# Kernel tuning notes

Measured on AMD Instinct MI355X. Metric: run time of the kernel, lower is better.

The kernel has to match this reference:

```python
import jax, jax.numpy as jnp
import numpy as np

T, H = 4096, 2048


def setup_inputs() -> dict:
    key = jax.random.key(0)
    k_a, k_b, k_x = jax.random.split(key, 3)
    # glorot-style init matching the module: uniform(-1,1) * sqrt(2/sum(shape))
    a = jax.random.uniform(k_a, (H,), minval=-1.0, maxval=1.0) * jnp.sqrt(2.0 / H)
    B = jax.random.uniform(k_b, (H, H), minval=-1.0, maxval=1.0) * jnp.sqrt(2.0 / (2 * H))
    x = jax.random.normal(k_x, (T, H), dtype=jnp.float32)
    return {"x": x, "a": a, "B": B}


def reference(x, a, B):
    # x: (T, H); per-timestep s_t = B.T @ x_t  ->  s = x @ B, laid out NCH = (1, H, T)
    Tl, Hl = x.shape
    s = jnp.einsum("th,hk->kt", x, B)[None]  # (1, H, T)
    # depthwise causal kernel: k[h, t] = a[h]**t, time as final dim, flipped for conv
    exponents = jnp.arange(Tl)
    kernel = jnp.power(a[:, None], exponents)          # (H, T)
    kernel_flipped = jnp.flip(kernel, axis=-1)[:, None, :]  # (H, 1, T) OIH
    s_padded = jnp.pad(s, ((0, 0), (0, 0), (Tl - 1, 0)))    # causal left-pad
    conv_out = jax.lax.conv_general_dilated(
        s_padded, kernel_flipped,
        window_strides=(1,), padding="VALID",
        dimension_numbers=("NCH", "OIH", "NCH"),
        feature_group_count=Hl,
    )  # (1, H, T): h_t[h] = sum_{k<=t} a[h]**(t-k) * s_k[h]
    return jnp.transpose(conv_out, (0, 2, 1))  # (1, T, H)
```

## Files before the change

kernel.cpp:

```cpp
#include <hip/hip_runtime.h>
#include <stdint.h>

#define TDIM 4096
#define HDIM 2048

#define BM 256
#define BN 128
#define BK 64
#define NKT (HDIM / BK)
#define AREG  34816
#define PERBUF 51200
#define SSTR   132

typedef short short8 __attribute__((ext_vector_type(8)));
typedef float f32x4 __attribute__((ext_vector_type(4)));

__device__ __forceinline__ uint16_t f2bf(float f) {
  uint32_t u = __builtin_bit_cast(uint32_t, f);
  u += 0x7fffu + ((u >> 16) & 1u);
  return (uint16_t)(u >> 16);
}
__device__ __forceinline__ float bf2f(uint32_t h) {
  uint32_t u = h << 16;
  return __builtin_bit_cast(float, u);
}

__device__ __forceinline__ void async_copy16(const void* gsrc, void* ldst) {
  __builtin_amdgcn_global_load_lds(
      (const __attribute__((address_space(1))) uint32_t*)gsrc,
      (__attribute__((address_space(3))) uint32_t*)ldst,
      16, 0, 0);
}

__global__ void prep(const float* __restrict__ x, const float* __restrict__ B,
                     uint16_t* __restrict__ xb, uint16_t* __restrict__ Bt) {
  __shared__ uint16_t tile[64][68];
  const int t = threadIdx.x;
  if (blockIdx.x < 4096) {
    size_t i = ((size_t)blockIdx.x * 256 + t) * 8;
    float4 v0 = *(const float4*)(x + i);
    float4 v1 = *(const float4*)(x + i + 4);
    union { uint16_t h[8]; uint4 v; } o;
    o.h[0] = f2bf(v0.x); o.h[1] = f2bf(v0.y); o.h[2] = f2bf(v0.z); o.h[3] = f2bf(v0.w);
    o.h[4] = f2bf(v1.x); o.h[5] = f2bf(v1.y); o.h[6] = f2bf(v1.z); o.h[7] = f2bf(v1.w);
    *(uint4*)(xb + i) = o.v;
  } else {
    const int bid = blockIdx.x - 4096;
    const int n0 = (bid & 31) * 64;
    const int k0 = (bid >> 5) * 64;
    {
      const int r  = t >> 4;
      const int c4 = (t & 15) * 4;
#pragma unroll
      for (int i = 0; i < 4; ++i) {
        int rr = r + i * 16;
        float4 v = *(const float4*)&B[(size_t)(k0 + rr) * HDIM + n0 + c4];
        union { uint16_t h[4]; uint2 u; } o;
        o.h[0] = f2bf(v.x); o.h[1] = f2bf(v.y); o.h[2] = f2bf(v.z); o.h[3] = f2bf(v.w);
        *(uint2*)&tile[rr][c4] = o.u;
      }
    }
    __syncthreads();
    {
      const int nr = t >> 2;
      const int kc = (t & 3) * 4;
#pragma unroll
      for (int i = 0; i < 4; ++i) {
        int kk = kc + i * 16;
        union { uint16_t h[4]; uint2 u; } o;
        o.h[0] = tile[kk][nr];     o.h[1] = tile[kk + 1][nr];
        o.h[2] = tile[kk + 2][nr]; o.h[3] = tile[kk + 3][nr];
        *(uint2*)&Bt[(size_t)(n0 + nr) * HDIM + k0 + kk] = o.u;
      }
    }
  }
}

__global__ __launch_bounds__(512, 2) void gemm_scan(
    const uint16_t* __restrict__ A, const uint16_t* __restrict__ Bt,
    const float* __restrict__ a, float* __restrict__ out) {
  __shared__ __align__(16) char lds[2 * PERBUF];

  const int tid  = threadIdx.x;
  const int lane = tid & 63;
  const int wave = tid >> 6;
  const int wm = (wave >> 1) * 64;
  const int wn = (wave & 1) * 64;

  const int flat = blockIdx.y * gridDim.x + blockIdx.x;
  const int logi = (flat & 7) * 32 + (flat >> 3);
  const int m0 = (logi >> 4) * BM;
  const int n0 = (logi & 15) * BN;

  f32x4 acc[4][4] = {};
  f32x4 accw[4] = {};

  const int lr = lane >> 3;
  const int gc = (lane & 7) ^ lr;

  const int fr = lane & 15;
  const int fq = lane >> 4;

  auto issue_tile = [&](int kt2) {
    size_t koff = (size_t)kt2 * (BK * 2);
    char* dst = lds + (kt2 & 1) * PERBUF;
#pragma unroll
    for (int i = 0; i < 4; ++i) {
      int g = wave * 4 + i;
      int row = m0 - 16 + g * 8 + lr;
      if (row < 0) row = 0;
      async_copy16((const char*)A + ((size_t)row * HDIM + gc * 8) * 2 + koff,
                   dst + g * 1024);
    }
    if (wave < 2) {
      int g = 32 + wave;
      int row = m0 - 16 + g * 8 + lr;
      async_copy16((const char*)A + ((size_t)row * HDIM + gc * 8) * 2 + koff,
                   dst + g * 1024);
    }
#pragma unroll
    for (int i = 0; i < 2; ++i) {
      int g = wave * 2 + i;
      int row = n0 + g * 8 + lr;
      async_copy16((const char*)Bt + ((size_t)row * HDIM + gc * 8) * 2 + koff,
                   dst + AREG + g * 1024);
    }
  };

  issue_tile(0);
  for (int kt = 0; kt < NKT; ++kt) {
    if (kt + 1 < NKT) {
      issue_tile(kt + 1);
      if (wave < 2) asm volatile("s_waitcnt vmcnt(7)" ::: "memory");
      else          asm volatile("s_waitcnt vmcnt(6)" ::: "memory");
    } else {
      asm volatile("s_waitcnt vmcnt(0)" ::: "memory");
    }
    asm volatile("s_barrier" ::: "memory");

    const char* base = lds + (kt & 1) * PERBUF;
#pragma unroll
    for (int s = 0; s < 2; ++s) {
      short8 af[4], bfr[4], aw;
#pragma unroll
      for (int im = 0; im < 4; ++im) {
        int row = 16 + wm + im * 16 + fr;
        af[im] = *(const short8*)(base + row * 128 + (((s * 4 + fq) ^ (fr & 7)) * 16));
      }
#pragma unroll
      for (int in = 0; in < 4; ++in) {
        int row = wn + in * 16 + fr;
        bfr[in] = *(const short8*)(base + AREG + row * 128 + (((s * 4 + fq) ^ (fr & 7)) * 16));
      }
#pragma unroll
      for (int im = 0; im < 4; ++im)
#pragma unroll
        for (int in = 0; in < 4; ++in)
          acc[im][in] = __builtin_amdgcn_mfma_f32_16x16x32_bf16(
              af[im], bfr[in], acc[im][in], 0, 0, 0);
      if (wave < 2) {
        aw = *(const short8*)(base + fr * 128 + (((s * 4 + fq) ^ (fr & 7)) * 16));
#pragma unroll
        for (int in = 0; in < 4; ++in)
          accw[in] = __builtin_amdgcn_mfma_f32_16x16x32_bf16(
              aw, bfr[in], accw[in], 0, 0, 0);
      }
    }

    asm volatile("s_barrier" ::: "memory");
  }

  uint16_t* Sl = (uint16_t*)lds;
#pragma unroll
  for (int im = 0; im < 4; ++im)
#pragma unroll
    for (int in = 0; in < 4; ++in)
#pragma unroll
      for (int r = 0; r < 4; ++r)
        Sl[(16 + wm + im * 16 + fq * 4 + r) * SSTR + wn + in * 16 + fr] =
            f2bf(acc[im][in][r]);
  if (wave < 2) {
#pragma unroll
    for (int in = 0; in < 4; ++in)
#pragma unroll
      for (int r = 0; r < 4; ++r)
        Sl[(fq * 4 + r) * SSTR + wn + in * 16 + fr] = f2bf(accw[in][r]);
  }
  __syncthreads();

  const int col   = tid & 127;
  const int chunk = tid >> 7;
  const float av  = a[n0 + col];
  float h = 0.f;
  if (!(m0 == 0 && chunk == 0)) {
#pragma unroll
    for (int i = 0; i < 16; ++i)
      h = av * h + bf2f(Sl[(chunk * 64 + i) * SSTR + col]);
  }
  float* op = out + (size_t)(m0 + chunk * 64) * HDIM + n0 + col;
#pragma unroll
  for (int i = 0; i < 64; ++i) {
    h = av * h + bf2f(Sl[(chunk * 64 + 16 + i) * SSTR + col]);
    op[(size_t)i * HDIM] = h;
  }
}

extern "C" void kernel_launch(void* const* d_in, const int* in_sizes, int n_in,
                              void* d_out, int out_size, void* d_ws, size_t ws_size,
                              hipStream_t stream) {
  const float* x = (const float*)d_in[0];
  const float* a = (const float*)d_in[1];
  const float* B = (const float*)d_in[2];
  float* out = (float*)d_out;

  uint16_t* xb  = (uint16_t*)d_ws;
  uint16_t* Btb = (uint16_t*)((char*)d_ws + (size_t)16 * 1024 * 1024);

  prep<<<4096 + 1024, 256, 0, stream>>>(x, B, xb, Btb);
  gemm_scan<<<dim3(HDIM / BN, TDIM / BM), 512, 0, stream>>>(xb, Btb, a, out);
}
```

Measured before the change: 137.3 us.

## Split A/B tile prefetch across K half-steps and add MFMA priority scheduling

The GEMM main loop now splits the prefetch of the next K tile. The A rows are issued at the top of the iteration and the B rows midway, after the second half's LDS fragments are read. One of the two barriers per iteration is moved to gate this, and each wave waits for `lgkmcnt(0)` ahead of an MFMA burst run at raised wave priority (`s_setprio`). The aim is to spread global-to-LDS traffic more evenly against the MFMA work and to cut barrier stalls. The bf16 transpose in the prep kernel now writes 16-byte vectors with a padded tile stride. In exchange, the buffer reuse now relies on subtler wait-count and barrier ordering, which risks LDS write-after-read races.

```diff
diff --git a/kernel.cpp b/kernel.cpp
--- a/kernel.cpp
+++ b/kernel.cpp
@@ -34,7 +34,7 @@
 
 __global__ void prep(const float* __restrict__ x, const float* __restrict__ B,
                      uint16_t* __restrict__ xb, uint16_t* __restrict__ Bt) {
-  __shared__ uint16_t tile[64][68];
+  __shared__ uint16_t tile[64][70];
   const int t = threadIdx.x;
   if (blockIdx.x < 4096) {
     size_t i = ((size_t)blockIdx.x * 256 + t) * 8;
@@ -62,15 +62,15 @@
     }
     __syncthreads();
     {
-      const int nr = t >> 2;
-      const int kc = (t & 3) * 4;
-#pragma unroll
-      for (int i = 0; i < 4; ++i) {
-        int kk = kc + i * 16;
-        union { uint16_t h[4]; uint2 u; } o;
-        o.h[0] = tile[kk][nr];     o.h[1] = tile[kk + 1][nr];
-        o.h[2] = tile[kk + 2][nr]; o.h[3] = tile[kk + 3][nr];
-        *(uint2*)&Bt[(size_t)(n0 + nr) * HDIM + k0 + kk] = o.u;
+      const int nr8 = t >> 3;
+      const int kc8 = (t & 7) * 8;
+#pragma unroll
+      for (int i = 0; i < 2; ++i) {
+        int nr = nr8 + i * 32;
+        union { uint16_t h[8]; uint4 v; } o;
+#pragma unroll
+        for (int j = 0; j < 8; ++j) o.h[j] = tile[kc8 + j][nr];
+        *(uint4*)&Bt[(size_t)(n0 + nr) * HDIM + k0 + kc8] = o.v;
       }
     }
   }
@@ -101,7 +101,7 @@
   const int fr = lane & 15;
   const int fq = lane >> 4;
 
-  auto issue_tile = [&](int kt2) {
+  auto issue_A = [&](int kt2) {
     size_t koff = (size_t)kt2 * (BK * 2);
     char* dst = lds + (kt2 & 1) * PERBUF;
 #pragma unroll
@@ -112,46 +112,54 @@
       async_copy16((const char*)A + ((size_t)row * HDIM + gc * 8) * 2 + koff,
                    dst + g * 1024);
     }
+  };
+  auto issue_B = [&](int kt2) {
+    size_t koff = (size_t)kt2 * (BK * 2);
+    char* dst = lds + (kt2 & 1) * PERBUF;
+#pragma unroll
+    for (int i = 0; i < 2; ++i) {
+      int g = wave * 2 + i;
+      int row = n0 + g * 8 + lr;
+      async_copy16((const char*)Bt + ((size_t)row * HDIM + gc * 8) * 2 + koff,
+                   dst + AREG + g * 1024);
+    }
     if (wave < 2) {
       int g = 32 + wave;
       int row = m0 - 16 + g * 8 + lr;
       async_copy16((const char*)A + ((size_t)row * HDIM + gc * 8) * 2 + koff,
                    dst + g * 1024);
     }
-#pragma unroll
-    for (int i = 0; i < 2; ++i) {
-      int g = wave * 2 + i;
-      int row = n0 + g * 8 + lr;
-      async_copy16((const char*)Bt + ((size_t)row * HDIM + gc * 8) * 2 + koff,
-                   dst + AREG + g * 1024);
-    }
   };
 
-  issue_tile(0);
+  issue_A(0);
+  issue_B(0);
+
   for (int kt = 0; kt < NKT; ++kt) {
+    const char* base = lds + (kt & 1) * PERBUF;
+
     if (kt + 1 < NKT) {
-      issue_tile(kt + 1);
-      if (wave < 2) asm volatile("s_waitcnt vmcnt(7)" ::: "memory");
-      else          asm volatile("s_waitcnt vmcnt(6)" ::: "memory");
+      issue_A(kt + 1);
+      asm volatile("s_waitcnt vmcnt(4)" ::: "memory");
     } else {
       asm volatile("s_waitcnt vmcnt(0)" ::: "memory");
     }
     asm volatile("s_barrier" ::: "memory");
-
-    const char* base = lds + (kt & 1) * PERBUF;
-#pragma unroll
-    for (int s = 0; s < 2; ++s) {
-      short8 af[4], bfr[4], aw;
-#pragma unroll
-      for (int im = 0; im < 4; ++im) {
-        int row = 16 + wm + im * 16 + fr;
-        af[im] = *(const short8*)(base + row * 128 + (((s * 4 + fq) ^ (fr & 7)) * 16));
-      }
-#pragma unroll
-      for (int in = 0; in < 4; ++in) {
-        int row = wn + in * 16 + fr;
-        bfr[in] = *(const short8*)(base + AREG + row * 128 + (((s * 4 + fq) ^ (fr & 7)) * 16));
-      }
+    {
+      short8 af[4], bfr[4];
+#pragma unroll
+      for (int im = 0; im < 4; ++im)
+        af[im] = *(const short8*)(base + (16 + wm + im * 16 + fr) * 128 +
+                                  ((fq ^ (fr & 7)) * 16));
+#pragma unroll
+      for (int in = 0; in < 4; ++in)
+        bfr[in] = *(const short8*)(base + AREG + (wn + in * 16 + fr) * 128 +
+                                   ((fq ^ (fr & 7)) * 16));
+      short8 aw = af[0];
+      if (wave < 2)
+        aw = *(const short8*)(base + fr * 128 + ((fq ^ (fr & 7)) * 16));
+      asm volatile("s_waitcnt lgkmcnt(0)" ::: "memory");
+      __builtin_amdgcn_sched_barrier(0);
+      __builtin_amdgcn_s_setprio(1);
 #pragma unroll
       for (int im = 0; im < 4; ++im)
 #pragma unroll
@@ -159,16 +167,49 @@
           acc[im][in] = __builtin_amdgcn_mfma_f32_16x16x32_bf16(
               af[im], bfr[in], acc[im][in], 0, 0, 0);
       if (wave < 2) {
-        aw = *(const short8*)(base + fr * 128 + (((s * 4 + fq) ^ (fr & 7)) * 16));
 #pragma unroll
         for (int in = 0; in < 4; ++in)
           accw[in] = __builtin_amdgcn_mfma_f32_16x16x32_bf16(
               aw, bfr[in], accw[in], 0, 0, 0);
       }
-    }
-
-    asm volatile("s_barrier" ::: "memory");
-  }
+      __builtin_amdgcn_s_setprio(0);
+    }
+
+    {
+      short8 af[4], bfr[4];
+#pragma unroll
+      for (int im = 0; im < 4; ++im)
+        af[im] = *(const short8*)(base + (16 + wm + im * 16 + fr) * 128 +
+                                  (((4 + fq) ^ (fr & 7)) * 16));
+#pragma unroll
+      for (int in = 0; in < 4; ++in)
+        bfr[in] = *(const short8*)(base + AREG + (wn + in * 16 + fr) * 128 +
+                                   (((4 + fq) ^ (fr & 7)) * 16));
+      short8 aw = af[0];
+      if (wave < 2)
+        aw = *(const short8*)(base + fr * 128 + (((4 + fq) ^ (fr & 7)) * 16));
+      if (kt + 1 < NKT) issue_B(kt + 1);
+      asm volatile("s_barrier" ::: "memory");
+      asm volatile("s_waitcnt lgkmcnt(0)" ::: "memory");
+      __builtin_amdgcn_sched_barrier(0);
+      __builtin_amdgcn_s_setprio(1);
+#pragma unroll
+      for (int im = 0; im < 4; ++im)
+#pragma unroll
+        for (int in = 0; in < 4; ++in)
+          acc[im][in] = __builtin_amdgcn_mfma_f32_16x16x32_bf16(
+              af[im], bfr[in], acc[im][in], 0, 0, 0);
+      if (wave < 2) {
+#pragma unroll
+        for (int in = 0; in < 4; ++in)
+          accw[in] = __builtin_amdgcn_mfma_f32_16x16x32_bf16(
+              aw, bfr[in], accw[in], 0, 0, 0);
+      }
+      __builtin_amdgcn_s_setprio(0);
+    }
+  }
+
+  __syncthreads();
 
   uint16_t* Sl = (uint16_t*)lds;
 #pragma unroll
```

New measurement: 137.2 us (median of 2 runs). About the same (-0.0%).

## Load A fragments directly to registers, stage only B through LDS

Applied to the files above, without the earlier changes.

The GEMM now loads the A operand fragments straight from global memory into registers, double-buffered across k-steps, and only B goes through LDS via async copies. This cuts LDS capacity and LDS read traffic per tile. MFMA blocks are also wrapped in setprio and a sched_barrier. The prep transpose is changed to write 16-byte vectors. The trade-offs are more VGPRs and global loads whose layout is less coalesced (16-byte chunks per lane across rows), plus tighter vmcnt accounting.

```diff
diff --git a/kernel.cpp b/kernel.cpp
--- a/kernel.cpp
+++ b/kernel.cpp
@@ -8,9 +8,8 @@
 #define BN 128
 #define BK 64
 #define NKT (HDIM / BK)
-#define AREG  34816
-#define PERBUF 51200
-#define SSTR   132
+#define BBUF  16384
+#define SSTR  132
 
 typedef short short8 __attribute__((ext_vector_type(8)));
 typedef float f32x4 __attribute__((ext_vector_type(4)));
@@ -34,7 +33,7 @@
 
 __global__ void prep(const float* __restrict__ x, const float* __restrict__ B,
                      uint16_t* __restrict__ xb, uint16_t* __restrict__ Bt) {
-  __shared__ uint16_t tile[64][68];
+  __shared__ uint16_t tile[64][70];
   const int t = threadIdx.x;
   if (blockIdx.x < 4096) {
     size_t i = ((size_t)blockIdx.x * 256 + t) * 8;
@@ -62,15 +61,15 @@
     }
     __syncthreads();
     {
-      const int nr = t >> 2;
-      const int kc = (t & 3) * 4;
-#pragma unroll
-      for (int i = 0; i < 4; ++i) {
-        int kk = kc + i * 16;
-        union { uint16_t h[4]; uint2 u; } o;
-        o.h[0] = tile[kk][nr];     o.h[1] = tile[kk + 1][nr];
-        o.h[2] = tile[kk + 2][nr]; o.h[3] = tile[kk + 3][nr];
-        *(uint2*)&Bt[(size_t)(n0 + nr) * HDIM + k0 + kk] = o.u;
+      const int nr8 = t >> 3;
+      const int kc8 = (t & 7) * 8;
+#pragma unroll
+      for (int i = 0; i < 2; ++i) {
+        int nr = nr8 + i * 32;
+        union { uint16_t h[8]; uint4 v; } o;
+#pragma unroll
+        for (int j = 0; j < 8; ++j) o.h[j] = tile[kc8 + j][nr];
+        *(uint4*)&Bt[(size_t)(n0 + nr) * HDIM + k0 + kc8] = o.v;
       }
     }
   }
@@ -79,7 +78,7 @@
 __global__ __launch_bounds__(512, 2) void gemm_scan(
     const uint16_t* __restrict__ A, const uint16_t* __restrict__ Bt,
     const float* __restrict__ a, float* __restrict__ out) {
-  __shared__ __align__(16) char lds[2 * PERBUF];
+  __shared__ __align__(16) char lds[71808];
 
   const int tid  = threadIdx.x;
   const int lane = tid & 63;
@@ -101,74 +100,88 @@
   const int fr = lane & 15;
   const int fq = lane >> 4;
 
-  auto issue_tile = [&](int kt2) {
+  const char* abase = (const char*)A +
+      ((size_t)(m0 + wm + fr) * HDIM + fq * 8) * 2;
+  int wrow = m0 - 16 + fr; if (wrow < 0) wrow = 0;
+  const char* wbase = (const char*)A + ((size_t)wrow * HDIM + fq * 8) * 2;
+
+  auto issueB = [&](int kt2, char* dst) {
     size_t koff = (size_t)kt2 * (BK * 2);
-    char* dst = lds + (kt2 & 1) * PERBUF;
-#pragma unroll
-    for (int i = 0; i < 4; ++i) {
-      int g = wave * 4 + i;
-      int row = m0 - 16 + g * 8 + lr;
-      if (row < 0) row = 0;
-      async_copy16((const char*)A + ((size_t)row * HDIM + gc * 8) * 2 + koff,
-                   dst + g * 1024);
-    }
-    if (wave < 2) {
-      int g = 32 + wave;
-      int row = m0 - 16 + g * 8 + lr;
-      async_copy16((const char*)A + ((size_t)row * HDIM + gc * 8) * 2 + koff,
-                   dst + g * 1024);
-    }
 #pragma unroll
     for (int i = 0; i < 2; ++i) {
       int g = wave * 2 + i;
       int row = n0 + g * 8 + lr;
       async_copy16((const char*)Bt + ((size_t)row * HDIM + gc * 8) * 2 + koff,
-                   dst + AREG + g * 1024);
+                   dst + g * 1024);
     }
   };
-
-  issue_tile(0);
-  for (int kt = 0; kt < NKT; ++kt) {
+  auto loadA = [&](int kt2, short8 (&nxt)[4][2], short8 (&awn)[2]) {
+    size_t koff = (size_t)kt2 * 128;
+#pragma unroll
+    for (int im = 0; im < 4; ++im) {
+      nxt[im][0] = *(const short8*)(abase + (size_t)im * 16 * HDIM * 2 + koff);
+      nxt[im][1] = *(const short8*)(abase + (size_t)im * 16 * HDIM * 2 + koff + 64);
+    }
+    if (wave < 2) {
+      awn[0] = *(const short8*)(wbase + koff);
+      awn[1] = *(const short8*)(wbase + koff + 64);
+    }
+  };
+
+  short8 rA[4][2], rB[4][2], awA[2], awB[2];
+  char* buf0 = lds;
+  char* buf1 = lds + BBUF;
+
+  auto body = [&](int kt, short8 (&cur)[4][2], short8 (&nxt)[4][2],
+                  short8 (&awc)[2], short8 (&awn)[2],
+                  char* curbuf, char* nxtbuf) {
     if (kt + 1 < NKT) {
-      issue_tile(kt + 1);
-      if (wave < 2) asm volatile("s_waitcnt vmcnt(7)" ::: "memory");
-      else          asm volatile("s_waitcnt vmcnt(6)" ::: "memory");
+      loadA(kt + 1, nxt, awn);
+      issueB(kt + 1, nxtbuf);
+      if (wave < 2) asm volatile("s_waitcnt vmcnt(12)" ::: "memory");
+      else          asm volatile("s_waitcnt vmcnt(10)" ::: "memory");
     } else {
       asm volatile("s_waitcnt vmcnt(0)" ::: "memory");
     }
     asm volatile("s_barrier" ::: "memory");
 
-    const char* base = lds + (kt & 1) * PERBUF;
 #pragma unroll
     for (int s = 0; s < 2; ++s) {
-      short8 af[4], bfr[4], aw;
-#pragma unroll
-      for (int im = 0; im < 4; ++im) {
-        int row = 16 + wm + im * 16 + fr;
-        af[im] = *(const short8*)(base + row * 128 + (((s * 4 + fq) ^ (fr & 7)) * 16));
-      }
-#pragma unroll
-      for (int in = 0; in < 4; ++in) {
-        int row = wn + in * 16 + fr;
-        bfr[in] = *(const short8*)(base + AREG + row * 128 + (((s * 4 + fq) ^ (fr & 7)) * 16));
-      }
+      short8 bfr[4];
+#pragma unroll
+      for (int in = 0; in < 4; ++in)
+        bfr[in] = *(const short8*)(curbuf + (wn + in * 16 + fr) * 128 +
+                                   (((s * 4 + fq) ^ (fr & 7)) * 16));
+      asm volatile("s_waitcnt lgkmcnt(0)" ::: "memory");
+      __builtin_amdgcn_sched_barrier(0);
+      __builtin_amdgcn_s_setprio(1);
 #pragma unroll
       for (int im = 0; im < 4; ++im)
 #pragma unroll
         for (int in = 0; in < 4; ++in)
           acc[im][in] = __builtin_amdgcn_mfma_f32_16x16x32_bf16(
-              af[im], bfr[in], acc[im][in], 0, 0, 0);
+              cur[im][s], bfr[in], acc[im][in], 0, 0, 0);
       if (wave < 2) {
-        aw = *(const short8*)(base + fr * 128 + (((s * 4 + fq) ^ (fr & 7)) * 16));
 #pragma unroll
         for (int in = 0; in < 4; ++in)
           accw[in] = __builtin_amdgcn_mfma_f32_16x16x32_bf16(
-              aw, bfr[in], accw[in], 0, 0, 0);
+              awc[s], bfr[in], accw[in], 0, 0, 0);
       }
-    }
-
+      __builtin_amdgcn_s_setprio(0);
+    }
     asm volatile("s_barrier" ::: "memory");
-  }
+  };
+
+  loadA(0, rA, awA);
+  issueB(0, buf0);
+
+#pragma unroll 1
+  for (int it = 0; it < NKT / 2; ++it) {
+    body(2 * it,     rA, rB, awA, awB, buf0, buf1);
+    body(2 * it + 1, rB, rA, awB, awA, buf1, buf0);
+  }
+
+  __syncthreads();
 
   uint16_t* Sl = (uint16_t*)lds;
 #pragma unroll
```

After: 180.7 us. +31.6%, slower.
